# Kernel tuning notes

Hardware: AMD Instinct MI355X
Metric: run time of the kernel (lower is better)

The kernel has to match this reference:

```python
import jax, jax.numpy as jnp
import numpy as np

DIM = 512
SEARCH = 8
RETRIEVAL = 8
HD = DIM // SEARCH      # head_dim = 64
HVD = DIM // RETRIEVAL  # head_v_dim = 64


def setup_inputs() -> dict:
    key = jax.random.key(0)
    ks = jax.random.split(key, 8)
    b, n = 4, 2048
    s = 0.02
    f32 = jnp.float32
    return {
        "x":   jax.random.normal(ks[0], (b, n, DIM), f32),
        "Wq":  jax.random.normal(ks[1], (DIM, DIM), f32) * s, "bq": jnp.zeros((DIM,), f32),
        "Wk":  jax.random.normal(ks[2], (DIM, DIM), f32) * s, "bk": jnp.zeros((DIM,), f32),
        "Wv":  jax.random.normal(ks[3], (DIM, DIM), f32) * s, "bv": jnp.zeros((DIM,), f32),
        "Wvq": jax.random.normal(ks[4], (DIM, DIM), f32) * s, "bvq": jnp.zeros((DIM,), f32),
        "Wvk": jax.random.normal(ks[5], (HVD, HD), f32) * s,  "bvk": jnp.zeros((HD,), f32),
        "Wo":  jax.random.normal(ks[6], (SEARCH * HVD, DIM), f32) * s, "bo": jnp.zeros((DIM,), f32),
    }


def reference(x, Wq, bq, Wk, bk, Wv, bv, Wvq, bvq, Wvk, bvk, Wo, bo):
    b, n, _ = x.shape
    scaling = HD ** -0.5
    # Stage 1: search attention with diagonal exclusion
    q = (x @ Wq + bq).reshape(b, n, SEARCH, HD) * scaling
    k = (x @ Wk + bk).reshape(b, n, SEARCH, HD)
    v = (x @ Wv + bv).reshape(b, n, RETRIEVAL, HVD)
    score = jnp.einsum('bnsh,bmsh->bsnm', q, k)           # [b,S,n,n]
    eye = jnp.eye(n, dtype=bool)
    score = jnp.where(eye, -jnp.inf, score)               # mask self-attention
    score = jax.nn.softmax(score, axis=-1)
    # Every search head attends over every retrieval value head
    out = jnp.einsum('bsnm,bmrv->bnsrv', score, v)        # [b,n,S,R,HVD]
    # Stage 2: gated retrieval selection
    q_v = (x @ Wvq + bvq).reshape(b, n, SEARCH, HD) * scaling
    k_v = out @ Wvk + bvk                                 # [b,n,S,R,HD]
    v_logits = jnp.einsum('bnsh,bnsrh->bnsr', q_v, k_v)   # [b,n,S,R]
    v_score = jax.nn.softmax(v_logits, axis=-1)
    out2 = jnp.einsum('bnsr,bnsrv->bnsv', v_score, out).reshape(b, n, SEARCH * HVD)
    y = out2 @ Wo + bo                                    # [b,n,DIM]
    return (y, score[:, :, None], v_score[..., None])
```

## Files before the change

### kernel.cpp

```cpp
#include <hip/hip_runtime.h>
#include <stdint.h>


typedef __bf16 bf16;
typedef __attribute__((ext_vector_type(8))) __bf16 bf16x8;
typedef __attribute__((ext_vector_type(4))) float f32x4;

__device__ __forceinline__ bf16 f2bf(float f) {
  unsigned u = __builtin_bit_cast(unsigned, f);
  unsigned r = (u + 0x7FFFu + ((u >> 16) & 1u)) >> 16;
  unsigned short h = (unsigned short)r;
  return __builtin_bit_cast(bf16, h);
}

__device__ __forceinline__ void gload16(const void* g, void* l) {
  __builtin_amdgcn_global_load_lds(
      (const __attribute__((address_space(1))) unsigned int*)g,
      (__attribute__((address_space(3))) unsigned int*)l, 16, 0, 0);
}

__global__ __launch_bounds__(256) void k_cvt_x(const float* __restrict__ x,
                                               bf16* __restrict__ xb) {
  long i = ((long)blockIdx.x * 256 + threadIdx.x) * 8;
  float4 a = *(const float4*)(x + i);
  float4 b = *(const float4*)(x + i + 4);
  bf16x8 o;
  o[0] = f2bf(a.x); o[1] = f2bf(a.y); o[2] = f2bf(a.z); o[3] = f2bf(a.w);
  o[4] = f2bf(b.x); o[5] = f2bf(b.y); o[6] = f2bf(b.z); o[7] = f2bf(b.w);
  *(bf16x8*)(xb + i) = o;
}

__global__ __launch_bounds__(256) void k_cvt_wcat(
    const float* __restrict__ Wq, const float* __restrict__ bq,
    const float* __restrict__ Wk, const float* __restrict__ bk,
    const float* __restrict__ Wv, const float* __restrict__ bv,
    const float* __restrict__ Wvq, const float* __restrict__ bvq,
    bf16* __restrict__ WcatT, float* __restrict__ bcat) {
  int j = blockIdx.x;
  int grp = j >> 9, jc = j & 511;
  const float* W; const float* bb; float sc;
  if (grp == 0)      { W = Wq;  bb = bq;  sc = 0.125f; }
  else if (grp == 1) { W = Wk;  bb = bk;  sc = 1.0f;   }
  else if (grp == 2) { W = Wv;  bb = bv;  sc = 1.0f;   }
  else               { W = Wvq; bb = bvq; sc = 0.125f; }
  for (int k = threadIdx.x; k < 512; k += 256)
    WcatT[j * 512 + k] = f2bf(W[k * 512 + jc] * sc);
  if (threadIdx.x == 0) bcat[j] = bb[jc] * sc;
}

__global__ __launch_bounds__(256) void k_cvt_wo(const float* __restrict__ Wo,
                                                bf16* __restrict__ WoT) {
  int j = blockIdx.x;
  for (int k = threadIdx.x; k < 512; k += 256)
    WoT[j * 512 + k] = f2bf(Wo[k * 512 + j]);
}

__global__ __launch_bounds__(256) void k_transpose_v(const bf16* __restrict__ qkvq,
                                                     bf16* __restrict__ vt) {
  __shared__ bf16 tile[64][72];
  int bidx = blockIdx.x;
  int ntile = bidx & 31, jt = (bidx >> 5) & 7, b = bidx >> 8;
  int tid = threadIdx.x;
  int r = tid >> 3, c8 = (tid & 7) * 8;
#pragma unroll
  for (int rr = r; rr < 64; rr += 32) {
    const bf16* src = qkvq + (long)(b * 2048 + ntile * 64 + rr) * 2048 + 1024 + jt * 64 + c8;
    bf16x8 v = *(const bf16x8*)src;
#pragma unroll
    for (int e = 0; e < 8; e++) tile[rr][c8 + e] = v[e];
  }
  __syncthreads();
#pragma unroll
  for (int rr = r; rr < 64; rr += 32) {
    bf16x8 v;
#pragma unroll
    for (int e = 0; e < 8; e++) v[e] = tile[c8 + e][rr];
    *(bf16x8*)(vt + ((long)b * 512 + jt * 64 + rr) * 2048 + ntile * 64 + c8) = v;
  }
}

__device__ __forceinline__ void cstore(float* p, float v) { *p = v; }
__device__ __forceinline__ void cstore(bf16* p, float v) { *p = f2bf(v); }

template <typename CT>
__global__ __launch_bounds__(256) void k_gemm(
    const bf16* __restrict__ A, int lda,
    const bf16* __restrict__ BT, int ldb,
    CT* __restrict__ C, int ldc,
    const float* __restrict__ bias,
    int K, int ntiles) {
  __shared__ bf16 smem[32 * 512];
  int mt = blockIdx.x / ntiles, nt = blockIdx.x % ntiles;
  int tid = threadIdx.x, lane = tid & 63, w = tid >> 6;
  int lr = lane & 15, lq = lane >> 4;
  int wm = w & 1, wn = w >> 1;

  f32x4 acc[4][4];
#pragma unroll
  for (int i = 0; i < 4; i++)
#pragma unroll
    for (int j = 0; j < 4; j++) acc[i][j] = (f32x4){0.f, 0.f, 0.f, 0.f};

  for (int k0 = 0; k0 < K; k0 += 64) {
#pragma unroll
    for (int ss = 0; ss < 8; ss++) {
      int gsl = w * 8 + ss;
      int sl = gsl & 15, g = sl >> 1, t = sl & 1;
      const bf16* src = (gsl < 16)
          ? A + (long)(mt * 128 + g * 16 + lr) * lda + k0 + t * 32 + lq * 8
          : BT + (long)(nt * 128 + g * 16 + lr) * ldb + k0 + t * 32 + lq * 8;
      gload16(src, &smem[gsl * 512]);
    }
    __syncthreads();
#pragma unroll
    for (int t = 0; t < 2; t++) {
      bf16x8 af[4], bfr[4];
#pragma unroll
      for (int i = 0; i < 4; i++)
        af[i] = *(const bf16x8*)&smem[((wm * 4 + i) * 2 + t) * 512 + lane * 8];
#pragma unroll
      for (int j = 0; j < 4; j++)
        bfr[j] = *(const bf16x8*)&smem[(16 + (wn * 4 + j) * 2 + t) * 512 + lane * 8];
#pragma unroll
      for (int i = 0; i < 4; i++)
#pragma unroll
        for (int j = 0; j < 4; j++)
          acc[i][j] = __builtin_amdgcn_mfma_f32_16x16x32_bf16(af[i], bfr[j], acc[i][j], 0, 0, 0);
    }
    __syncthreads();
  }
#pragma unroll
  for (int i = 0; i < 4; i++) {
    int row = mt * 128 + wm * 64 + i * 16 + lq * 4;
#pragma unroll
    for (int j = 0; j < 4; j++) {
      int col = nt * 128 + wn * 64 + j * 16 + lr;
      float bv_ = bias[col];
#pragma unroll
      for (int r = 0; r < 4; r++)
        cstore(C + (long)(row + r) * ldc + col, acc[i][j][r] + bv_);
    }
  }
}

__global__ __launch_bounds__(256) void k_rowsum(const bf16* __restrict__ qkvq,
                                                float* __restrict__ rinv) {
  __shared__ bf16 smem[32 * 512];
  int rt = blockIdx.x & 15, s = (blockIdx.x >> 4) & 7, b = blockIdx.x >> 7;
  int tid = threadIdx.x, lane = tid & 63, w = tid >> 6;
  int lr = lane & 15, lq = lane >> 4;
  const bf16* Q = qkvq + (long)b * 2048 * 2048 + s * 64;
  const bf16* Kp = qkvq + (long)b * 2048 * 2048 + 512 + s * 64;

#pragma unroll
  for (int ss = 0; ss < 4; ss++) {
    int sl = w * 4 + ss, g = sl >> 1, t = sl & 1;
    gload16(Q + (long)(rt * 128 + g * 16 + lr) * 2048 + t * 32 + lq * 8, &smem[sl * 512]);
  }
  float racc[2][4];
#pragma unroll
  for (int i = 0; i < 2; i++)
#pragma unroll
    for (int r = 0; r < 4; r++) racc[i][r] = 0.f;

  for (int mt = 0; mt < 16; mt++) {
#pragma unroll
    for (int ss = 0; ss < 4; ss++) {
      int sl = w * 4 + ss, g = sl >> 1, t = sl & 1;
      gload16(Kp + (long)(mt * 128 + g * 16 + lr) * 2048 + t * 32 + lq * 8,
              &smem[(16 + sl) * 512]);
    }
    __syncthreads();
    f32x4 acc[2][8];
#pragma unroll
    for (int i = 0; i < 2; i++)
#pragma unroll
      for (int j = 0; j < 8; j++) acc[i][j] = (f32x4){0.f, 0.f, 0.f, 0.f};
#pragma unroll
    for (int t = 0; t < 2; t++) {
      bf16x8 af[2], bfr[8];
#pragma unroll
      for (int i = 0; i < 2; i++)
        af[i] = *(const bf16x8*)&smem[((w * 2 + i) * 2 + t) * 512 + lane * 8];
#pragma unroll
      for (int j = 0; j < 8; j++)
        bfr[j] = *(const bf16x8*)&smem[(16 + j * 2 + t) * 512 + lane * 8];
#pragma unroll
      for (int i = 0; i < 2; i++)
#pragma unroll
        for (int j = 0; j < 8; j++)
          acc[i][j] = __builtin_amdgcn_mfma_f32_16x16x32_bf16(af[i], bfr[j], acc[i][j], 0, 0, 0);
    }
#pragma unroll
    for (int i = 0; i < 2; i++) {
      int gnb = rt * 128 + w * 32 + i * 16 + lq * 4;
#pragma unroll
      for (int j = 0; j < 8; j++) {
        int gm = mt * 128 + j * 16 + lr;
#pragma unroll
        for (int r = 0; r < 4; r++) {
          float e = __expf(acc[i][j][r]);
          racc[i][r] += (gm == gnb + r) ? 0.f : e;
        }
      }
    }
    __syncthreads();
  }
#pragma unroll
  for (int i = 0; i < 2; i++)
#pragma unroll
    for (int r = 0; r < 4; r++) {
      float v = racc[i][r];
      v += __shfl_xor(v, 1); v += __shfl_xor(v, 2);
      v += __shfl_xor(v, 4); v += __shfl_xor(v, 8);
      if (lr == 0)
        rinv[(long)(b * 8 + s) * 2048 + rt * 128 + w * 32 + i * 16 + lq * 4 + r] = 1.0f / v;
    }
}

__global__ __launch_bounds__(256) void k_pwrite(const bf16* __restrict__ qkvq,
                                                const float* __restrict__ rinv,
                                                float* __restrict__ scout) {
  __shared__ bf16 smem[32 * 512];
  __shared__ float rl[128];
  int mt = blockIdx.x & 15, rt = (blockIdx.x >> 4) & 15;
  int s = (blockIdx.x >> 8) & 7, b = blockIdx.x >> 11;
  int tid = threadIdx.x, lane = tid & 63, w = tid >> 6;
  int lr = lane & 15, lq = lane >> 4;
  int wm = w & 1, wn = w >> 1;
  const bf16* Q = qkvq + (long)b * 2048 * 2048 + s * 64;
  const bf16* Kp = qkvq + (long)b * 2048 * 2048 + 512 + s * 64;

#pragma unroll
  for (int ss = 0; ss < 8; ss++) {
    int gsl = w * 8 + ss;
    int sl = gsl & 15, g = sl >> 1, t = sl & 1;
    const bf16* src = (gsl < 16)
        ? Q + (long)(rt * 128 + g * 16 + lr) * 2048 + t * 32 + lq * 8
        : Kp + (long)(mt * 128 + g * 16 + lr) * 2048 + t * 32 + lq * 8;
    gload16(src, &smem[gsl * 512]);
  }
  if (tid < 128) rl[tid] = rinv[(long)(b * 8 + s) * 2048 + rt * 128 + tid];
  __syncthreads();

  f32x4 acc[4][4];
#pragma unroll
  for (int i = 0; i < 4; i++)
#pragma unroll
    for (int j = 0; j < 4; j++) acc[i][j] = (f32x4){0.f, 0.f, 0.f, 0.f};
#pragma unroll
  for (int t = 0; t < 2; t++) {
    bf16x8 af[4], bfr[4];
#pragma unroll
    for (int i = 0; i < 4; i++)
      af[i] = *(const bf16x8*)&smem[((wm * 4 + i) * 2 + t) * 512 + lane * 8];
#pragma unroll
    for (int j = 0; j < 4; j++)
      bfr[j] = *(const bf16x8*)&smem[(16 + (wn * 4 + j) * 2 + t) * 512 + lane * 8];
#pragma unroll
    for (int i = 0; i < 4; i++)
#pragma unroll
      for (int j = 0; j < 4; j++)
        acc[i][j] = __builtin_amdgcn_mfma_f32_16x16x32_bf16(af[i], bfr[j], acc[i][j], 0, 0, 0);
  }
  float* outp = scout + ((long)(b * 8 + s) * 2048 + rt * 128) * 2048 + mt * 128;
#pragma unroll
  for (int i = 0; i < 4; i++) {
    int rowl = wm * 64 + i * 16 + lq * 4;
#pragma unroll
    for (int j = 0; j < 4; j++) {
      int col = wn * 64 + j * 16 + lr;
      int gm = mt * 128 + col;
#pragma unroll
      for (int r = 0; r < 4; r++) {
        int rrow = rowl + r;
        int gn = rt * 128 + rrow;
        float p = (gm == gn) ? 0.f : __expf(acc[i][j][r]) * rl[rrow];
        outp[(long)rrow * 2048 + col] = p;
      }
    }
  }
}

__global__ __launch_bounds__(256) void k_pv(const float* __restrict__ P,
                                            const bf16* __restrict__ vt,
                                            bf16* __restrict__ out1) {
  __shared__ bf16 smem[32 * 512];
  int id = (blockIdx.x & 7) * 256 + (blockIdx.x >> 3);
  int nt = id & 3, mt = (id >> 2) & 15;
  int s = (id >> 6) & 7, b = id >> 9;
  int tid = threadIdx.x, lane = tid & 63, w = tid >> 6;
  int lr = lane & 15, lq = lane >> 4;
  int wm = w & 1, wn = w >> 1;
  const float* Pb = P + (long)(b * 8 + s) * 2048 * 2048;
  const bf16* Vb = vt + (long)b * 512 * 2048;

  f32x4 acc[4][4];
#pragma unroll
  for (int i = 0; i < 4; i++)
#pragma unroll
    for (int j = 0; j < 4; j++) acc[i][j] = (f32x4){0.f, 0.f, 0.f, 0.f};

  for (int k0 = 0; k0 < 2048; k0 += 64) {
#pragma unroll
    for (int ss = 0; ss < 4; ss++) {
      int sl = w * 4 + ss, g = sl >> 1, t = sl & 1;
      gload16(Vb + (long)(nt * 128 + g * 16 + lr) * 2048 + k0 + t * 32 + lq * 8,
              &smem[(16 + sl) * 512]);
    }
#pragma unroll
    for (int ss = 0; ss < 4; ss++) {
      int sl = w * 4 + ss, g = sl >> 1, t = sl & 1;
      const float* src = Pb + (long)(mt * 128 + g * 16 + lr) * 2048 + k0 + t * 32 + lq * 8;
      float4 x0 = *(const float4*)src;
      float4 x1 = *(const float4*)(src + 4);
      bf16x8 o;
      o[0] = f2bf(x0.x); o[1] = f2bf(x0.y); o[2] = f2bf(x0.z); o[3] = f2bf(x0.w);
      o[4] = f2bf(x1.x); o[5] = f2bf(x1.y); o[6] = f2bf(x1.z); o[7] = f2bf(x1.w);
      *(bf16x8*)&smem[sl * 512 + lane * 8] = o;
    }
    __syncthreads();
#pragma unroll
    for (int t = 0; t < 2; t++) {
      bf16x8 af[4], bfr[4];
#pragma unroll
      for (int i = 0; i < 4; i++)
        af[i] = *(const bf16x8*)&smem[((wm * 4 + i) * 2 + t) * 512 + lane * 8];
#pragma unroll
      for (int j = 0; j < 4; j++)
        bfr[j] = *(const bf16x8*)&smem[(16 + (wn * 4 + j) * 2 + t) * 512 + lane * 8];
#pragma unroll
      for (int i = 0; i < 4; i++)
#pragma unroll
        for (int j = 0; j < 4; j++)
          acc[i][j] = __builtin_amdgcn_mfma_f32_16x16x32_bf16(af[i], bfr[j], acc[i][j], 0, 0, 0);
    }
    __syncthreads();
  }
  bf16* Ob = out1 + (long)(b * 8 + s) * 2048 * 512;
#pragma unroll
  for (int i = 0; i < 4; i++) {
    int row = mt * 128 + wm * 64 + i * 16 + lq * 4;
#pragma unroll
    for (int j = 0; j < 4; j++) {
      int col = nt * 128 + wn * 64 + j * 16 + lr;
#pragma unroll
      for (int r = 0; r < 4; r++)
        Ob[(long)(row + r) * 512 + col] = f2bf(acc[i][j][r]);
    }
  }
}

__global__ __launch_bounds__(256) void k_stage2(const bf16* __restrict__ out1,
                                                const bf16* __restrict__ qkvq,
                                                const float* __restrict__ Wvk,
                                                float* __restrict__ vsout,
                                                bf16* __restrict__ out2) {
  __shared__ float so[8][8][64];
  __shared__ float qvl[4][2][64];
  int b = blockIdx.x >> 11, n = blockIdx.x & 2047;
  int tid = threadIdx.x, w = tid >> 6, lane = tid & 63;

  float wr[64];
#pragma unroll
  for (int c = 0; c < 16; c++) {
    float4 t4 = *(const float4*)(Wvk + lane * 64 + c * 4);
    wr[c * 4 + 0] = t4.x; wr[c * 4 + 1] = t4.y;
    wr[c * 4 + 2] = t4.z; wr[c * 4 + 3] = t4.w;
  }
  for (int c = tid; c < 512; c += 256) {
    int s = c >> 6; int off = (c & 63) * 8;
    bf16x8 v = *(const bf16x8*)(out1 + ((long)(b * 8 + s) * 2048 + n) * 512 + off);
#pragma unroll
    for (int e = 0; e < 8; e++) so[s][(off + e) >> 6][(off + e) & 63] = (float)v[e];
  }
#pragma unroll
  for (int si = 0; si < 2; si++) {
    int s = w * 2 + si;
    qvl[w][si][lane] = (float)qkvq[(long)(b * 2048 + n) * 2048 + 1536 + s * 64 + lane];
  }
  __syncthreads();

#pragma unroll
  for (int si = 0; si < 2; si++) {
    int s = w * 2 + si;
    float qw = 0.f;
#pragma unroll
    for (int c = 0; c < 16; c++) {
      float4 q4 = *(const float4*)&qvl[w][si][c * 4];
      qw += q4.x * wr[c * 4 + 0] + q4.y * wr[c * 4 + 1] +
            q4.z * wr[c * 4 + 2] + q4.w * wr[c * 4 + 3];
    }
    float lg[8], sor[8];
#pragma unroll
    for (int r = 0; r < 8; r++) {
      sor[r] = so[s][r][lane];
      float p = sor[r] * qw;
      p += __shfl_xor(p, 1);  p += __shfl_xor(p, 2);  p += __shfl_xor(p, 4);
      p += __shfl_xor(p, 8);  p += __shfl_xor(p, 16); p += __shfl_xor(p, 32);
      lg[r] = p;
    }
    float mx = lg[0];
#pragma unroll
    for (int r = 1; r < 8; r++) mx = fmaxf(mx, lg[r]);
    float e[8], sum = 0.f;
#pragma unroll
    for (int r = 0; r < 8; r++) { e[r] = __expf(lg[r] - mx); sum += e[r]; }
    float rs = 1.f / sum;
    float myv = 0.f;
#pragma unroll
    for (int r = 0; r < 8; r++) myv = (lane == r) ? e[r] * rs : myv;
    if (lane < 8) vsout[((long)(b * 2048 + n) * 8 + s) * 8 + lane] = myv;
    float o2 = 0.f;
#pragma unroll
    for (int r = 0; r < 8; r++) o2 += e[r] * rs * sor[r];
    out2[(long)(b * 2048 + n) * 512 + s * 64 + lane] = f2bf(o2);
  }
}

extern "C" void kernel_launch(void* const* d_in, const int* in_sizes, int n_in,
                              void* d_out, int out_size, void* d_ws, size_t ws_size,
                              hipStream_t stream) {
  const float* x   = (const float*)d_in[0];
  const float* Wq  = (const float*)d_in[1];  const float* bq  = (const float*)d_in[2];
  const float* Wk  = (const float*)d_in[3];  const float* bk  = (const float*)d_in[4];
  const float* Wv  = (const float*)d_in[5];  const float* bv  = (const float*)d_in[6];
  const float* Wvq = (const float*)d_in[7];  const float* bvq = (const float*)d_in[8];
  const float* Wvk = (const float*)d_in[9];  const float* bvk = (const float*)d_in[10];
  const float* Wo  = (const float*)d_in[11]; const float* bo  = (const float*)d_in[12];
  (void)bvk; (void)in_sizes; (void)n_in; (void)out_size; (void)ws_size;

  char* ws = (char*)d_ws;
  bf16*  qkvq  = (bf16*)(ws + 0);
  bf16*  xb    = (bf16*)(ws + 33554432);
  bf16*  wcatT = (bf16*)(ws + 41943040);
  bf16*  woT   = (bf16*)(ws + 44040192);
  float* bcat  = (float*)(ws + 44564480);
  bf16*  vt    = (bf16*)(ws + 44572672);
  float* rinv  = (float*)(ws + 52961280);
  bf16*  out1  = (bf16*)(ws + 53223424);
  bf16*  out2  = (bf16*)(ws + 120332288);

  float* y  = (float*)d_out;
  float* sc = y + 4194304;
  float* vs = y + 138412032;

  k_cvt_x<<<2048, 256, 0, stream>>>(x, xb);
  k_cvt_wcat<<<2048, 256, 0, stream>>>(Wq, bq, Wk, bk, Wv, bv, Wvq, bvq, wcatT, bcat);
  k_cvt_wo<<<512, 256, 0, stream>>>(Wo, woT);
  k_gemm<bf16><<<1024, 256, 0, stream>>>(xb, 512, wcatT, 512, qkvq, 2048, bcat, 512, 16);
  k_transpose_v<<<1024, 256, 0, stream>>>(qkvq, vt);
  k_rowsum<<<512, 256, 0, stream>>>(qkvq, rinv);
  k_pwrite<<<8192, 256, 0, stream>>>(qkvq, rinv, sc);
  k_pv<<<2048, 256, 0, stream>>>(sc, vt, out1);
  k_stage2<<<8192, 256, 0, stream>>>(out1, qkvq, Wvk, vs, out2);
  k_gemm<float><<<256, 256, 0, stream>>>(out2, 512, woT, 512, y, 512, bo, 512, 4);
}
```

Baseline: 1.170 ms.

## Write bf16 copy of probabilities and feed PV matmul from it

```diff
diff --git a/kernel.cpp b/kernel.cpp
--- a/kernel.cpp
+++ b/kernel.cpp
@@ -220,7 +220,8 @@
 
 __global__ __launch_bounds__(256) void k_pwrite(const bf16* __restrict__ qkvq,
                                                 const float* __restrict__ rinv,
-                                                float* __restrict__ scout) {
+                                                float* __restrict__ scout,
+                                                bf16* __restrict__ pb) {
   __shared__ bf16 smem[32 * 512];
   __shared__ float rl[128];
   int mt = blockIdx.x & 15, rt = (blockIdx.x >> 4) & 15;
@@ -263,7 +264,9 @@
       for (int j = 0; j < 4; j++)
         acc[i][j] = __builtin_amdgcn_mfma_f32_16x16x32_bf16(af[i], bfr[j], acc[i][j], 0, 0, 0);
   }
-  float* outp = scout + ((long)(b * 8 + s) * 2048 + rt * 128) * 2048 + mt * 128;
+  long pbase = ((long)(b * 8 + s) * 2048 + rt * 128) * 2048 + mt * 128;
+  float* outp = scout + pbase;
+  bf16* pbp = pb ? pb + pbase : (bf16*)0;
 #pragma unroll
   for (int i = 0; i < 4; i++) {
     int rowl = wm * 64 + i * 16 + lq * 4;
@@ -277,7 +280,69 @@
         int gn = rt * 128 + rrow;
         float p = (gm == gn) ? 0.f : __expf(acc[i][j][r]) * rl[rrow];
         outp[(long)rrow * 2048 + col] = p;
+        if (pbp) pbp[(long)rrow * 2048 + col] = f2bf(p);
       }
+    }
+  }
+}
+
+__global__ __launch_bounds__(256) void k_pv_bf(const bf16* __restrict__ Pb,
+                                               const bf16* __restrict__ vt,
+                                               bf16* __restrict__ out1) {
+  __shared__ bf16 smem[32 * 512];
+  int id = (blockIdx.x & 7) * 256 + (blockIdx.x >> 3);
+  int nt = id & 3, mt = (id >> 2) & 15;
+  int s = (id >> 6) & 7, b = id >> 9;
+  int tid = threadIdx.x, lane = tid & 63, w = tid >> 6;
+  int lr = lane & 15, lq = lane >> 4;
+  int wm = w & 1, wn = w >> 1;
+  const bf16* A = Pb + (long)(b * 8 + s) * 2048 * 2048;
+  const bf16* BT = vt + (long)b * 512 * 2048;
+
+  f32x4 acc[4][4];
+#pragma unroll
+  for (int i = 0; i < 4; i++)
+#pragma unroll
+    for (int j = 0; j < 4; j++) acc[i][j] = (f32x4){0.f, 0.f, 0.f, 0.f};
+
+  for (int k0 = 0; k0 < 2048; k0 += 64) {
+#pragma unroll
+    for (int ss = 0; ss < 8; ss++) {
+      int gsl = w * 8 + ss;
+      int sl = gsl & 15, g = sl >> 1, t = sl & 1;
+      const bf16* src = (gsl < 16)
+          ? A + (long)(mt * 128 + g * 16 + lr) * 2048 + k0 + t * 32 + lq * 8
+          : BT + (long)(nt * 128 + g * 16 + lr) * 2048 + k0 + t * 32 + lq * 8;
+      gload16(src, &smem[gsl * 512]);
+    }
+    __syncthreads();
+#pragma unroll
+    for (int t = 0; t < 2; t++) {
+      bf16x8 af[4], bfr[4];
+#pragma unroll
+      for (int i = 0; i < 4; i++)
+        af[i] = *(const bf16x8*)&smem[((wm * 4 + i) * 2 + t) * 512 + lane * 8];
+#pragma unroll
+      for (int j = 0; j < 4; j++)
+        bfr[j] = *(const bf16x8*)&smem[(16 + (wn * 4 + j) * 2 + t) * 512 + lane * 8];
+#pragma unroll
+      for (int i = 0; i < 4; i++)
+#pragma unroll
+        for (int j = 0; j < 4; j++)
+          acc[i][j] = __builtin_amdgcn_mfma_f32_16x16x32_bf16(af[i], bfr[j], acc[i][j], 0, 0, 0);
+    }
+    __syncthreads();
+  }
+  bf16* Ob = out1 + (long)(b * 8 + s) * 2048 * 512;
+#pragma unroll
+  for (int i = 0; i < 4; i++) {
+    int row = mt * 128 + wm * 64 + i * 16 + lq * 4;
+#pragma unroll
+    for (int j = 0; j < 4; j++) {
+      int col = nt * 128 + wn * 64 + j * 16 + lr;
+#pragma unroll
+      for (int r = 0; r < 4; r++)
+        Ob[(long)(row + r) * 512 + col] = f2bf(acc[i][j][r]);
     }
   }
 }
@@ -428,7 +493,7 @@
   const float* Wvq = (const float*)d_in[7];  const float* bvq = (const float*)d_in[8];
   const float* Wvk = (const float*)d_in[9];  const float* bvk = (const float*)d_in[10];
   const float* Wo  = (const float*)d_in[11]; const float* bo  = (const float*)d_in[12];
-  (void)bvk; (void)in_sizes; (void)n_in; (void)out_size; (void)ws_size;
+  (void)bvk; (void)in_sizes; (void)n_in; (void)out_size;
 
   char* ws = (char*)d_ws;
   bf16*  qkvq  = (bf16*)(ws + 0);
@@ -440,6 +505,8 @@
   float* rinv  = (float*)(ws + 52961280);
   bf16*  out1  = (bf16*)(ws + 53223424);
   bf16*  out2  = (bf16*)(ws + 120332288);
+  bool big = ws_size >= 397156352UL;
+  bf16* pb = big ? (bf16*)(ws + 128720896) : (bf16*)0;
 
   float* y  = (float*)d_out;
   float* sc = y + 4194304;
@@ -451,8 +518,9 @@
   k_gemm<bf16><<<1024, 256, 0, stream>>>(xb, 512, wcatT, 512, qkvq, 2048, bcat, 512, 16);
   k_transpose_v<<<1024, 256, 0, stream>>>(qkvq, vt);
   k_rowsum<<<512, 256, 0, stream>>>(qkvq, rinv);
-  k_pwrite<<<8192, 256, 0, stream>>>(qkvq, rinv, sc);
-  k_pv<<<2048, 256, 0, stream>>>(sc, vt, out1);
+  k_pwrite<<<8192, 256, 0, stream>>>(qkvq, rinv, sc, pb);
+  if (big) k_pv_bf<<<2048, 256, 0, stream>>>(pb, vt, out1);
+  else     k_pv<<<2048, 256, 0, stream>>>(sc, vt, out1);
   k_stage2<<<8192, 256, 0, stream>>>(out1, qkvq, Wvk, vs, out2);
   k_gemm<float><<<256, 256, 0, stream>>>(out2, 512, woT, 512, y, 512, bo, 512, 4);
 }
```

After: 1.170 ms. About the same (-0.0%).
